# Kernel optimization log

Hardware: AMD Instinct MI355X
Metric: run time of the kernel (lower is better)

The kernel has to match this reference:

```python
import jax, jax.numpy as jnp
import numpy as np

N = 6144       # nodes
E = 98304      # edges (~16 per node)
D = 256        # input_dim
K = 20         # max_clusters
NUM_LVS = 32   # distinct LV group ids
MIN_SIZE = 3.0
MAX_SIZE = 20.0


def _lv_constraint_table():
    # Static per-LV preferred-cluster soft constraint (0.3 base, 1.0 preferred).
    max_cpl = max(2, K // max(1, NUM_LVS - 5))
    table = np.ones((NUM_LVS, K), dtype=np.float32)
    for i in range(NUM_LVS):
        start = (i * 2) % K
        end = min(start + max_cpl, K)
        pref = np.zeros(K, dtype=np.float32)
        pref[start:end] = 1.0
        table[i] = 0.3 + 0.7 * pref
    return jnp.asarray(table)

_LV_TABLE = _lv_constraint_table()


def _apply_size_constraints(S):
    cs = S.sum(axis=0)  # soft cluster sizes [K]
    pen = jnp.zeros_like(cs)
    pen = jnp.where(cs > MAX_SIZE, -jnp.log(cs / MAX_SIZE + 1e-8), pen)
    pen = jnp.where((cs > 0) & (cs < MIN_SIZE), -0.5 * jnp.log(cs / MIN_SIZE + 1e-8), pen)
    S_adj = jax.nn.softmax(jnp.log(S + 1e-8) + pen[None, :], axis=1)
    very_over = cs > MAX_SIZE * 1.5
    for k in range(K):  # K is small & static; sequential like the original
        col = S_adj[:, k]
        thr = jnp.quantile(col, 0.7)
        weak = (col < thr) & very_over[k]
        S_adj = S_adj.at[:, k].set(jnp.where(weak, 0.0, col))
        rs = jnp.sum(jnp.abs(S_adj), axis=1, keepdims=True)
        S_adj = jnp.where(weak[:, None], S_adj / jnp.maximum(rs, 1e-12), S_adj)
    return jnp.where(jnp.any(pen != 0.0), S_adj, S)


def _hard_rebalance(S):
    n = S.shape[0]
    for _ in range(5):  # fixed max_iterations (early-break is a no-op via masks)
        cs = S.sum(axis=0)  # stale within the k-loop, as in the original
        very_over = cs > MAX_SIZE
        for k in range(K):
            excess = cs[k] - MAX_SIZE
            active = very_over[k] & (excess > 0)
            col = S[:, k]
            num = jnp.minimum(jnp.ceil(excess).astype(jnp.int32) + 5, n)
            order = jnp.argsort(col)  # ascending: weakest first
            ranks = jnp.zeros((n,), jnp.int32).at[order].set(jnp.arange(n, dtype=jnp.int32))
            weak = (ranks < num) & active
            S = S.at[:, k].set(jnp.where(weak, 1e-8, col))
            avail = jnp.clip(MAX_SIZE - cs, 0.0, None)
            w = avail / (avail.sum() + 1e-8)
            S = jnp.where(weak[:, None], S + w[None, :] * S[:, k:k + 1], S)
            rs = jnp.sum(jnp.abs(S), axis=1, keepdims=True)
            S = jnp.where(weak[:, None], S / jnp.maximum(rs, 1e-12), S)
    return S


def _forward(x, edge_index, lv_group_ids, W1, b1, W2, b2, W3, b3, We1, be1, We2, be2):
    n = x.shape[0]
    # assign_net (dropout is identity in eval)
    h = jax.nn.relu(x @ W1 + b1)
    h = jax.nn.relu(h @ W2 + b2)
    logits = h @ W3 + b3  # [N, K]

    # LV mask: values in {0.3, 1.0}; masked_fill only triggers on exact zeros (kept faithful)
    lv_sizes = jax.ops.segment_sum(jnp.ones((n,), logits.dtype), lv_group_ids, num_segments=NUM_LVS)
    big = (lv_sizes > 30.0)[lv_group_ids]
    lv_mask = jnp.where(big[:, None], _LV_TABLE[lv_group_ids], 1.0)
    logits = jnp.where(lv_mask == 0.0, -1e9, logits)

    # load-balancing regularization (reconstructed; source truncated)
    S_soft = jax.nn.softmax(logits, axis=1)
    target = n / K
    logits = logits - 0.1 * (S_soft.sum(axis=0) - target)[None, :] / target

    S = jax.nn.softmax(logits, axis=1)
    S = _apply_size_constraints(S)
    S = _hard_rebalance(S)

    x_embed = jax.nn.relu(x @ We1 + be1) @ We2 + be2
    x_pooled = S.T @ x_embed  # [K, D]

    adj = jnp.zeros((n, n), x.dtype).at[edge_index[0], edge_index[1]].set(1.0)
    adj_pooled = S.T @ adj @ S  # [K, K]

    # link prediction loss: BCE(S S^T, adj) with torch's log clamp at -100
    p = jnp.clip(S @ S.T, 0.0, 1.0)
    logp = jnp.maximum(jnp.log(p), -100.0)
    log1mp = jnp.maximum(jnp.log1p(-p), -100.0)
    link_loss = -jnp.mean(adj * logp + (1.0 - adj) * log1mp)

    entropy_loss = -jnp.mean(jnp.sum(S * jnp.log(S + 1e-8), axis=1))
    balance_loss = jnp.mean(jnp.abs(S.sum(axis=0) - target)) / target
    aux = link_loss + 0.1 * entropy_loss + 0.5 * balance_loss
    return x_pooled, adj_pooled, S, aux


def setup_inputs() -> dict:
    key = jax.random.key(0)
    ks = jax.random.split(key, 8)
    x = jax.random.normal(ks[0], (N, D), jnp.float32)
    edge_index = jax.random.randint(ks[1], (2, E), 0, N)
    lv_group_ids = jax.random.randint(ks[2], (N,), 0, NUM_LVS)

    def lin(k, fi, fo):
        k1, k2 = jax.random.split(k)
        lim = 1.0 / np.sqrt(fi)
        return (jax.random.uniform(k1, (fi, fo), jnp.float32, -lim, lim),
                jax.random.uniform(k2, (fo,), jnp.float32, -lim, lim))

    W1, b1 = lin(ks[3], D, D // 2)
    W2, b2 = lin(ks[4], D // 2, D // 4)
    W3 = jax.random.normal(ks[5], (D // 4, K), jnp.float32) * 0.1  # _init_balanced_assignment
    b3 = jnp.zeros((K,), jnp.float32)
    We1, be1 = lin(ks[6], D, D)
    We2, be2 = lin(ks[7], D, D)
    return dict(x=x, edge_index=edge_index, lv_group_ids=lv_group_ids,
                W1=W1, b1=b1, W2=W2, b2=b2, W3=W3, b3=b3,
                We1=We1, be1=be1, We2=We2, be2=be2)


def reference(x, edge_index, lv_group_ids, W1, b1, W2, b2, W3, b3, We1, be1, We2, be2):
    return _forward(x, edge_index, lv_group_ids, W1, b1, W2, b2, W3, b3, We1, be1, We2, be2)
```

## Files before the change

kernel.cpp:

```cpp
#include <hip/hip_runtime.h>
#include <math.h>

#define N_NODES 6144
#define KCL 20
#define NE 98304
#define RPT 6

#define OFF_BITMAP   491520ull
#define OFF_COLSUM0  5210112ull
#define OFF_CSG      5210192ull
#define OFF_CSFIN    5210272ull
#define OFF_DACC     5210368ull
#define OFF_TICK     5210400ull
#define OFF_GBAR2    5210404ull
#define HDR_BYTES    296ull
#define OFF_LOGITS   5210624ull
#define OFF_WEAK     5235200ull
#define OFF_CSS      5358080ull
#define OFF_TOTZ     5358160ull
#define OFF_UCM      5702144ull
#define OFF_XE       6685184ull
#define OFF_GOUT     13001216ull
#define OFF_RWS      13025792ull

__global__ __launch_bounds__(128) void k_mlp(const float* __restrict__ x,
    const float* __restrict__ W1, const float* __restrict__ b1,
    const float* __restrict__ W2, const float* __restrict__ b2,
    const float* __restrict__ W3, const float* __restrict__ b3,
    float* __restrict__ logits, float* __restrict__ colsum0,
    unsigned* __restrict__ bitmap, float* __restrict__ outHead){
  __shared__ float xs[16][256];
  __shared__ float h1[16][128];
  __shared__ float h2[16][64];
  __shared__ float logitsL[16][20];
  __shared__ float csL[20];
  const int tid = threadIdx.x;
  const int r0 = blockIdx.x * 16;
  { uint4* bm4 = (uint4*)bitmap;
    const int base = blockIdx.x*128 + tid;
    const uint4 z = make_uint4(0u,0u,0u,0u);
    #pragma unroll
    for (int i=0;i<6;i++) bm4[base + i*49152] = z; }
  if (blockIdx.x==0){ for (int i=tid;i<5520;i+=128) outHead[i]=0.f; }
  if (tid < 20) csL[tid]=0.f;
  for (int idx = tid; idx < 16*256; idx += 128){ int u = idx >> 8, i = idx & 255; xs[u][i] = x[(r0+u)*256 + i]; }
  __syncthreads();
  {
    float acc[16]; float bb = b1[tid];
    #pragma unroll
    for (int u=0;u<16;u++) acc[u]=bb;
    for (int i=0;i<256;i++){ float wv = W1[i*128+tid];
      #pragma unroll
      for (int u=0;u<16;u++) acc[u]=fmaf(xs[u][i], wv, acc[u]); }
    #pragma unroll
    for (int u=0;u<16;u++) h1[u][tid]=fmaxf(acc[u],0.f);
  }
  __syncthreads();
  if (tid < 64){
    float acc[16]; float bb = b2[tid];
    #pragma unroll
    for (int u=0;u<16;u++) acc[u]=bb;
    for (int i=0;i<128;i++){ float wv = W2[i*64+tid];
      #pragma unroll
      for (int u=0;u<16;u++) acc[u]=fmaf(h1[u][i], wv, acc[u]); }
    #pragma unroll
    for (int u=0;u<16;u++) h2[u][tid]=fmaxf(acc[u],0.f);
  }
  __syncthreads();
  if (tid < 20){
    float acc[16]; float bb = b3[tid];
    #pragma unroll
    for (int u=0;u<16;u++) acc[u]=bb;
    for (int i=0;i<64;i++){ float wv = W3[i*20+tid];
      #pragma unroll
      for (int u=0;u<16;u++) acc[u]=fmaf(h2[u][i], wv, acc[u]); }
    #pragma unroll
    for (int u=0;u<16;u++){ logits[(r0+u)*20+tid]=acc[u]; logitsL[u][tid]=acc[u]; }
  }
  __syncthreads();
  if (tid < 16){
    float y[20]; float m=-INFINITY;
    #pragma unroll
    for (int c=0;c<20;c++){ y[c]=logitsL[tid][c]; m=fmaxf(m,y[c]); }
    float s=0.f;
    #pragma unroll
    for (int c=0;c<20;c++){ y[c]=expf(y[c]-m); s+=y[c]; }
    #pragma unroll
    for (int c=0;c<20;c++) atomicAdd(&csL[c], y[c]/s);
  }
  __syncthreads();
  if (tid < 20) atomicAdd(&colsum0[tid], csL[tid]);
}

__global__ __launch_bounds__(256) void k_sm2p(const float* __restrict__ logits,
    const float* __restrict__ colsum0, float* __restrict__ Ucm,
    float* __restrict__ csG, float* __restrict__ Rws, unsigned* __restrict__ gbar2){
  __shared__ float adjv[20]; __shared__ float csL[20];
  const int tid = threadIdx.x;
  if (tid < 20){ adjv[tid] = (0.1f*(colsum0[tid]-307.2f))/307.2f; csL[tid]=0.f; }
  __syncthreads();
  const int r = blockIdx.x*256 + tid;
  float y[20]; float m=-INFINITY;
  const float4* lp = (const float4*)(logits + r*20);
  #pragma unroll
  for (int q=0;q<5;q++){ float4 f=lp[q]; y[q*4]=f.x; y[q*4+1]=f.y; y[q*4+2]=f.z; y[q*4+3]=f.w; }
  #pragma unroll
  for (int c=0;c<20;c++){ y[c]=y[c]-adjv[c]; m=fmaxf(m,y[c]); }
  float s=0.f;
  #pragma unroll
  for (int c=0;c<20;c++){ y[c]=expf(y[c]-m); s+=y[c]; }
  #pragma unroll
  for (int c=0;c<20;c++){ float v=y[c]/s; y[c]=v; Ucm[c*6144+r]=v; atomicAdd(&csL[c], v); }
  __syncthreads();
  if (tid < 20) atomicAdd(&csG[tid], csL[tid]);
  __syncthreads();
  if (tid==0){
    __threadfence();
    __hip_atomic_fetch_add(gbar2, 1u, __ATOMIC_RELEASE, __HIP_MEMORY_SCOPE_AGENT);
    while (__hip_atomic_load(gbar2, __ATOMIC_ACQUIRE, __HIP_MEMORY_SCOPE_AGENT) < 24u)
      __builtin_amdgcn_s_sleep(2);
    __threadfence();
  }
  __syncthreads();
  float pen[20]; int flag=0;
  #pragma unroll
  for (int c=0;c<20;c++){ float cc=csG[c]; float p=0.f;
    if (cc > 20.0f) p = -logf(cc/20.0f + 1e-8f);
    if (cc > 0.0f && cc < 3.0f) p = -0.5f*logf(cc/3.0f + 1e-8f);
    pen[c]=p; if (p != 0.f) flag=1; }
  float ts=0.f;
  if (flag){
    float m2=-INFINITY;
    #pragma unroll
    for (int c=0;c<20;c++){ y[c]=logf(y[c]+1e-8f)+pen[c]; m2=fmaxf(m2,y[c]); }
    float s2=0.f;
    #pragma unroll
    for (int c=0;c<20;c++){ y[c]=expf(y[c]-m2); s2+=y[c]; }
    #pragma unroll
    for (int c=0;c<20;c++){ float vv=y[c]/s2; Ucm[c*6144+r]=vv; ts+=vv; }
  } else {
    #pragma unroll
    for (int c=0;c<20;c++) ts+=y[c];
  }
  Rws[r]=ts;
}


__device__ __forceinline__ void load6(const float* p, float* v){
  const float2* q = (const float2*)p;
  float2 a=q[0], b=q[1], c=q[2];
  v[0]=a.x; v[1]=a.y; v[2]=b.x; v[3]=b.y; v[4]=c.x; v[5]=c.y;
}

struct MidShared {
  unsigned hist[2048*8];
  unsigned pad[3000];
  double wred[16*20];
  int wT20[16][20]; int wB20[16][20]; int totZ20[20];
  float csGs[20]; float csS[20];
  unsigned st[8];
  alignas(16) unsigned wMin[16];
  alignas(16) int wS[16];
};

__device__ __forceinline__ int blockExclScan16(int val, int tid, int lane, int wv,
                                               int* wS, int* totOut){
  __syncthreads();
  int inc = val;
  for (int off=1;off<64;off<<=1){ int nv=__shfl_up(inc,off); if (lane>=off) inc+=nv; }
  if (lane==63) wS[wv]=inc;
  __syncthreads();
  int4 a=*(int4*)&wS[0], b=*(int4*)&wS[4], c=*(int4*)&wS[8], d=*(int4*)&wS[12];
  int tot = a.x+a.y+a.z+a.w + b.x+b.y+b.z+b.w + c.x+c.y+c.z+c.w + d.x+d.y+d.z+d.w;
  int base = 0;
  base += (wv> 0)?a.x:0; base += (wv> 1)?a.y:0; base += (wv> 2)?a.z:0; base += (wv> 3)?a.w:0;
  base += (wv> 4)?b.x:0; base += (wv> 5)?b.y:0; base += (wv> 6)?b.z:0; base += (wv> 7)?b.w:0;
  base += (wv> 8)?c.x:0; base += (wv> 9)?c.y:0; base += (wv>10)?c.z:0; base += (wv>11)?c.w:0;
  base += (wv>12)?d.x:0; base += (wv>13)?d.y:0; base += (wv>14)?d.z:0;
  *totOut = tot;
  return base + inc - val;
}

struct SelRes { unsigned kv, below, rankin, ties; };

__device__ SelRes selectKth6(const float* v, int rank0, unsigned* hist,
                             unsigned* st, int* wS, int tid, int lane, int wv){
  unsigned st0=0u, st1=0u, st2=(unsigned)rank0, st3=0u;
  const unsigned rep=(unsigned)(lane&7);
  bool done=false;
  for (int p=0;p<3 && !done;p++){
    const int shift=(p==0)?21:((p==1)?10:0);
    const int bins =(p==2)?1024:2048;
    unsigned bb[RPT];
    #pragma unroll
    for (int u=0;u<RPT;u++){
      unsigned key=__float_as_uint(v[u]);
      bool ok=(p==0);
      if (p==1) ok=((key>>21)==(st0>>21));
      if (p==2) ok=((key>>10)==(st0>>10));
      bb[u]= ok ? ((key>>shift)&(unsigned)(bins-1)) : 0xFFFFFFFFu;
    }
    #pragma unroll
    for (int u=0;u<RPT;u++){
      bool first=(bb[u]!=0xFFFFFFFFu);
      #pragma unroll
      for (int j=0;j<u;j++) first = first && (bb[j]!=bb[u]);
      if (first){
        unsigned cnt=1u;
        #pragma unroll
        for (int j=u+1;j<RPT;j++) cnt += (bb[j]==bb[u]) ? 1u:0u;
        atomicAdd(&hist[(bb[u]<<3)+rep], cnt);
      }
    }
    __syncthreads();
    const uint4 z4=make_uint4(0u,0u,0u,0u);
    unsigned bs0, bs1=0u, s;
    const unsigned b0=(unsigned)tid*(unsigned)(bins>>10);
    {
      uint4* h4=(uint4*)&hist[b0<<3];
      uint4 x0=h4[0],x1=h4[1];
      bs0=x0.x+x0.y+x0.z+x0.w + x1.x+x1.y+x1.z+x1.w;
      h4[0]=z4; h4[1]=z4;
      if (bins==2048){
        uint4 x2=h4[2],x3=h4[3];
        bs1=x2.x+x2.y+x2.z+x2.w + x3.x+x3.y+x3.z+x3.w;
        h4[2]=z4; h4[3]=z4;
      }
      s=bs0+bs1;
    }
    unsigned inc=s;
    for (int off=1;off<64;off<<=1){ unsigned nv=(unsigned)__shfl_up((int)inc,off); if (lane>=off) inc+=nv; }
    if (lane==63) wS[wv]=(int)inc;
    __syncthreads();
    int4 wa=*(int4*)&wS[0], wb=*(int4*)&wS[4], wc=*(int4*)&wS[8], wd=*(int4*)&wS[12];
    unsigned base=0u;
    base += (wv> 0)?(unsigned)wa.x:0u; base += (wv> 1)?(unsigned)wa.y:0u;
    base += (wv> 2)?(unsigned)wa.z:0u; base += (wv> 3)?(unsigned)wa.w:0u;
    base += (wv> 4)?(unsigned)wb.x:0u; base += (wv> 5)?(unsigned)wb.y:0u;
    base += (wv> 6)?(unsigned)wb.z:0u; base += (wv> 7)?(unsigned)wb.w:0u;
    base += (wv> 8)?(unsigned)wc.x:0u; base += (wv> 9)?(unsigned)wc.y:0u;
    base += (wv>10)?(unsigned)wc.z:0u; base += (wv>11)?(unsigned)wc.w:0u;
    base += (wv>12)?(unsigned)wd.x:0u; base += (wv>13)?(unsigned)wd.y:0u;
    base += (wv>14)?(unsigned)wd.z:0u;
    unsigned P=base+inc-s;
    if (P<=st2 && st2<P+s){
      unsigned run=P, bsel, hc;
      if (st2 < P+bs0){ bsel=b0;    hc=bs0; }
      else            { run=P+bs0; bsel=b0+1u; hc=bs1; }
      st[0]=st0|(bsel<<(unsigned)shift);
      st[1]=st1+run;
      st[2]=st2-run;
      st[3]=hc;
      st[4]=0xFFFFFFFFu;
      st[5]=0u;
    }
    __syncthreads();
    st0=st[0]; st1=st[1]; st2=st[2]; st3=st[3];
    if (p<2 && st3<=2u){
      #pragma unroll
      for (int u=0;u<RPT;u++){
        unsigned key=__float_as_uint(v[u]);
        if ((key>>(unsigned)shift)==(st0>>(unsigned)shift)){
          atomicMin(&st[4],key); atomicMax(&st[5],key);
        }
      }
      __syncthreads();
      unsigned kmin=st[4], kmax=st[5];
      if (st3==1u)            st0=kmin;
      else if (kmin==kmax)    st0=kmin;
      else if (st2==0u){      st0=kmin; st3=1u; }
      else             {      st0=kmax; st1+=1u; st2=0u; st3=1u; }
      done=true;
    }
  }
  SelRes r; r.kv=st0; r.below=st1; r.rankin=st2; r.ties=st3; return r;
}

__device__ void constr_block(MidShared& sm, const float* __restrict__ csG,
    float* __restrict__ Rws, float* __restrict__ G2, float* __restrict__ Ucm){
  unsigned* hist = sm.hist; unsigned* st = sm.st; int* wS = sm.wS;
  const int tid = threadIdx.x;
  const int lane = tid & 63, wv = tid >> 6;
  const int r0 = tid*RPT;

  { uint4* h4=(uint4*)hist; const uint4 z=make_uint4(0u,0u,0u,0u);
    #pragma unroll
    for (int i=0;i<4;i++) h4[tid+i*1024]=z; }
  if (tid<20) sm.csGs[tid]=csG[tid];
  __syncthreads();

  int flag=0;
  #pragma unroll
  for (int c=0;c<20;c++){ float cc=sm.csGs[c]; float p=0.f;
    if (cc > 20.0f) p = -logf(cc/20.0f + 1e-8f);
    if (cc > 0.0f && cc < 3.0f) p = -0.5f*logf(cc/3.0f + 1e-8f);
    if (p != 0.f) flag=1; }

  float G[RPT], R[RPT];
  load6(Rws + r0, R);
  #pragma unroll
  for (int u=0;u<RPT;u++) G[u]=1.0f;

  if (flag){
    float u24[RPT]; bool have=false;
    for (int k=0;k<20;k++){
      if (!(sm.csGs[k] > 30.0f)){ have=false; continue; }
      if (!have) load6(Ucm + k*6144 + r0, u24);
      float u24n[RPT];
      if (k<19) load6(Ucm + (k+1)*6144 + r0, u24n);
      float sv24[RPT];
      #pragma unroll
      for (int u=0;u<RPT;u++) sv24[u]=__fmul_rn(u24[u], G[u]);
      SelRes sr = selectKth6(sv24, 4300, hist, st, wS, tid, lane, wv);
      float vlo = __uint_as_float(sr.kv);
      float vhi;
      if (sr.rankin + 1u < sr.ties) vhi = vlo;
      else {
        unsigned kV = sr.kv;
        unsigned lm = 0xFFFFFFFFu;
        #pragma unroll
        for (int u=0;u<RPT;u++){ unsigned key=__float_as_uint(sv24[u]); if (key>kV && key<lm) lm=key; }
        for (int off=32;off>0;off>>=1){ unsigned o=(unsigned)__shfl_down((int)lm,off); if (o<lm) lm=o; }
        if (lane==0) sm.wMin[wv]=lm;
        __syncthreads();
        uint4 m0=*(uint4*)&sm.wMin[0], m1=*(uint4*)&sm.wMin[4];
        uint4 m2=*(uint4*)&sm.wMin[8], m3=*(uint4*)&sm.wMin[12];
        lm = m0.x; lm = (m0.y<lm)?m0.y:lm; lm = (m0.z<lm)?m0.z:lm; lm = (m0.w<lm)?m0.w:lm;
        lm = (m1.x<lm)?m1.x:lm; lm = (m1.y<lm)?m1.y:lm; lm = (m1.z<lm)?m1.z:lm; lm = (m1.w<lm)?m1.w:lm;
        lm = (m2.x<lm)?m2.x:lm; lm = (m2.y<lm)?m2.y:lm; lm = (m2.z<lm)?m2.z:lm; lm = (m2.w<lm)?m2.w:lm;
        lm = (m3.x<lm)?m3.x:lm; lm = (m3.y<lm)?m3.y:lm; lm = (m3.z<lm)?m3.z:lm; lm = (m3.w<lm)?m3.w:lm;
        vhi = __uint_as_float(lm);
      }
      float thr = __fadd_rn(__fmul_rn(vlo, 0.89990234375f), __fmul_rn(vhi, 0.10009765625f));
      #pragma unroll
      for (int u=0;u<RPT;u++){
        if (sv24[u] < thr){
          Ucm[k*6144+r0+u] = 0.0f;
          float rs  = __fsub_rn(__fmul_rn(R[u], G[u]), sv24[u]);
          float rsm = fmaxf(rs, 1e-12f);
          G[u] = __fdiv_rn(G[u], rsm);
          R[u] = __fsub_rn(R[u], u24[u]);
        }
      }
      #pragma unroll
      for (int u=0;u<RPT;u++) u24[u]=u24n[u];
      have = (k<19);
    }
  }

  { float2* gp = (float2*)(G2 + r0);
    gp[0]=make_float2(G[0],G[1]); gp[1]=make_float2(G[2],G[3]); gp[2]=make_float2(G[4],G[5]); }
  { float2* rp = (float2*)(Rws + r0);
    rp[0]=make_float2(R[0],R[1]); rp[1]=make_float2(R[2],R[3]); rp[2]=make_float2(R[4],R[5]); }
}

__device__ void embed_block(MidShared& sm, const float* __restrict__ x,
    const float* __restrict__ We1, const float* __restrict__ be1,
    const float* __restrict__ We2, const float* __restrict__ be2,
    float* __restrict__ xe, int blk){
  float (*xs)[256] = (float (*)[256])(sm.hist);
  float (*h)[256]  = (float (*)[256])(sm.hist + 4096);
  const int tid = threadIdx.x;
  const int col = tid & 255;
  const int ug  = tid >> 8;
  const int r0 = blk * 16;
  { float4* xsf4 = (float4*)xs;
    xsf4[tid] = ((const float4*)(x + r0*256))[tid]; }
  __syncthreads();
  float acc[4];
  { float bb = be1[col];
    #pragma unroll
    for (int u=0;u<4;u++) acc[u]=bb; }
  for (int i=0;i<256;i+=4){
    float w0 = We1[(i+0)*256+col];
    float w1 = We1[(i+1)*256+col];
    float w2 = We1[(i+2)*256+col];
    float w3 = We1[(i+3)*256+col];
    #pragma unroll
    for (int u=0;u<4;u++){
      const float4 xv = *(const float4*)&xs[ug*4+u][i];
      acc[u]=fmaf(xv.x, w0, acc[u]);
      acc[u]=fmaf(xv.y, w1, acc[u]);
      acc[u]=fmaf(xv.z, w2, acc[u]);
      acc[u]=fmaf(xv.w, w3, acc[u]);
    }
  }
  #pragma unroll
  for (int u=0;u<4;u++) h[ug*4+u][col]=fmaxf(acc[u],0.f);
  __syncthreads();
  { float bb = be2[col];
    #pragma unroll
    for (int u=0;u<4;u++) acc[u]=bb; }
  for (int i=0;i<256;i+=4){
    float w0 = We2[(i+0)*256+col];
    float w1 = We2[(i+1)*256+col];
    float w2 = We2[(i+2)*256+col];
    float w3 = We2[(i+3)*256+col];
    #pragma unroll
    for (int u=0;u<4;u++){
      const float4 xv = *(const float4*)&h[ug*4+u][i];
      acc[u]=fmaf(xv.x, w0, acc[u]);
      acc[u]=fmaf(xv.y, w1, acc[u]);
      acc[u]=fmaf(xv.z, w2, acc[u]);
      acc[u]=fmaf(xv.w, w3, acc[u]);
    }
  }
  #pragma unroll
  for (int u=0;u<4;u++) xe[(r0+ug*4+u)*256+col]=acc[u];
}

__global__ __launch_bounds__(1024) void k_midwide(const float* __restrict__ csG,
    float* __restrict__ Rws, float* __restrict__ G2,
    float* __restrict__ Ucm,
    const float* __restrict__ x,
    const float* __restrict__ We1, const float* __restrict__ be1,
    const float* __restrict__ We2, const float* __restrict__ be2,
    float* __restrict__ xe,
    const int* __restrict__ ei, unsigned int* __restrict__ bitmap){
  __shared__ MidShared sm;
  const int blk = blockIdx.x;
  if (blk == 0){
    constr_block(sm, csG, Rws, G2, Ucm);
  } else if (blk <= 384){
    embed_block(sm, x, We1, be1, We2, be2, xe, blk-1);
  } else {
    const int e = (blk-385)*1024 + threadIdx.x;
    const int i = ei[e], j = ei[NE+e];
    unsigned bit = (unsigned)i*6144u + (unsigned)j;
    atomicOr(&bitmap[bit >> 5], 1u << (bit & 31u));
  }
}

__global__ __launch_bounds__(1024) void k_rbA(const float* __restrict__ G2,
    const float* __restrict__ Ucm, float* __restrict__ csS, int* __restrict__ totZ,
    unsigned char* __restrict__ weakIt){
  __shared__ double wredL[16];
  __shared__ int wTL[16];
  const int c = blockIdx.x;
  const int tid = threadIdx.x;
  const int lane = tid & 63, wv = tid >> 6;
  const int r0 = tid*RPT;
  float vv[RPT], g[RPT];
  load6(Ucm + c*6144 + r0, vv);
  load6(G2 + r0, g);
  double d=0.0; int z=0;
  #pragma unroll
  for (int u=0;u<RPT;u++){
    if (vv[u]==0.0f) z++;
    d += (double)__fmul_rn(vv[u], g[u]);
  }
  for (int off=32;off>0;off>>=1) d += __shfl_down(d, off);
  int inc=z;
  for (int off=1;off<64;off<<=1){ int nv=__shfl_up(inc,off); if (lane>=off) inc+=nv; }
  if (lane==0)  wredL[wv]=d;
  if (lane==63) wTL[wv]=inc;
  __syncthreads();
  double s=0.0;
  #pragma unroll
  for (int w2=0;w2<16;w2++) s += wredL[w2];
  const float cs=(float)s;
  int base=0, tz=0;
  #pragma unroll
  for (int w2=0;w2<16;w2++){ int t=wTL[w2]; if (w2<wv) base+=t; tz+=t; }
  int num=(int)ceilf(cs-20.0f)+5; if (num>6144) num=6144;
  const bool act = (cs > 20.0f);
  int rank = base + inc - z;
  #pragma unroll
  for (int u=0;u<RPT;u++){
    bool zb = (vv[u]==0.0f);
    unsigned char wi = 255;
    if (act && zb && rank < 5*num) wi = (unsigned char)(rank / num);
    weakIt[c*6144 + r0 + u] = wi;
    if (zb) rank++;
  }
  if (tid==0){ csS[c]=cs; totZ[c]=tz; }
}

__global__ __launch_bounds__(1024) void k_rbB(const float* __restrict__ G2,
    const float* __restrict__ Rws, float* __restrict__ Ucm, float* __restrict__ Gout,
    const float* __restrict__ csS, const int* __restrict__ totZ,
    const unsigned char* __restrict__ weakIt){
  __shared__ MidShared sm;
  const int tid = threadIdx.x;
  float csL[20]; float s0=0.f; unsigned actm=0u;
  #pragma unroll
  for (int c=0;c<20;c++){ float cs=csS[c]; csL[c]=cs;
    s0 += fmaxf(20.0f-cs,0.f);
    if (cs > 20.0f) actm |= (1u<<c); }
  const int wzero=(s0==0.0f)?1:0;
  const float wsum=s0+1e-8f;
  const int anyA=(actm!=0u)?1:0;
  int fastok = wzero;
  #pragma unroll
  for (int c=0;c<20;c++){
    if ((actm>>c)&1u){
      int num=(int)ceilf(csL[c]-20.0f)+5; if (num>6144) num=6144;
      if (5*num > totZ[c]) fastok=0;
    }
  }
  if (!anyA){
    const int r = blockIdx.x*1024 + tid;
    Gout[r] = G2[r];
    return;
  }
  if (fastok){
    const int r = blockIdx.x*1024 + tid;
    float G=G2[r], R=Rws[r];
    unsigned char wi[20];
    #pragma unroll
    for (int c=0;c<20;c++) wi[c]=weakIt[c*6144+r];
    #pragma unroll
    for (int i=0;i<5;i++){
      #pragma unroll
      for (int c=0;c<20;c++){
        if (wi[c]==(unsigned char)i){
          float Gold = G;
          float t   = __fadd_rn(__fmul_rn(R, Gold), 1e-8f);
          float rsm = fmaxf(t, 1e-12f);
          float un  = __fdiv_rn(1e-8f, Gold);
          Ucm[c*6144+r] = un;
          G = __fdiv_rn(Gold, rsm);
          R = __fadd_rn(R, un);
        }
      }
    }
    Gout[r]=G;
  } else {
    if (blockIdx.x!=0) return;
    unsigned* hist = sm.hist; unsigned* st = sm.st; int* wS = sm.wS;
    const int lane = tid & 63, wv = tid >> 6;
    const int r0 = tid*RPT;
    { uint4* h4=(uint4*)hist; const uint4 z=make_uint4(0u,0u,0u,0u);
      #pragma unroll
      for (int i=0;i<4;i++) h4[tid+i*1024]=z; }
    __syncthreads();
    float G[RPT], R[RPT];
    load6(G2 + r0, G);
    load6(Rws + r0, R);
    for (int it=0; it<5; it++){
      int zb2[RPT];
      #pragma unroll
      for (int u=0;u<RPT;u++) zb2[u]=0;
      for (int c=0;c<20;c++){
        float vv[RPT];
        load6(Ucm + c*6144 + r0, vv);
        double d=0.0;
        #pragma unroll
        for (int u=0;u<RPT;u++){
          if (vv[u]==0.0f) zb2[u] |= (1<<c);
          d += (double)__fmul_rn(vv[u], G[u]);
        }
        for (int off=32;off>0;off>>=1) d += __shfl_down(d, off);
        if (lane==0) sm.wred[wv*20+c]=d;
      }
      __syncthreads();
      if (tid<20){ double s=0.0; for (int w2=0;w2<16;w2++) s += sm.wred[w2*20+tid]; sm.csS[tid]=(float)s; }
      __syncthreads();
      float t0=0.f; unsigned am=0u;
      #pragma unroll
      for (int c=0;c<20;c++){
        float cs=sm.csS[c];
        t0 += fmaxf(20.0f-cs,0.f);
        if (cs > 20.0f) am |= (1u<<c);
      }
      const int wz = (t0==0.0f) ? 1 : 0;
      const float ws2 = t0 + 1e-8f;
      int exc2[20];
      #pragma unroll
      for (int c=0;c<20;c++){
        int z=0;
        #pragma unroll
        for (int u=0;u<RPT;u++) z += (zb2[u]>>c)&1;
        int inc = z;
        for (int off=1;off<64;off<<=1){ int nv=__shfl_up(inc,off); if (lane>=off) inc+=nv; }
        if (lane==63) sm.wT20[wv][c]=inc;
        exc2[c]=inc-z;
      }
      __syncthreads();
      if (tid<20){
        int run=0;
        for (int w2=0;w2<16;w2++){ sm.wB20[w2][tid]=run; run+=sm.wT20[w2][tid]; }
        sm.totZ20[tid]=run;
      }
      __syncthreads();
      const int aa = (am!=0u) ? 1 : 0;
      int ng=0;
      #pragma unroll
      for (int c=0;c<20;c++){
        if ((am>>c)&1u){
          float cs=sm.csS[c];
          int num=(int)ceilf(cs-20.0f)+5; if (num>6144) num=6144;
          if (num > sm.totZ20[c]) ng=1;
        }
      }
      if (aa && !wz) ng=1;
      if (!aa) continue;
      if (!ng){
        #pragma unroll
        for (int c=0;c<20;c++){
          if ((am>>c)&1u){
            float cs=sm.csS[c];
            int num=(int)ceilf(cs-20.0f)+5; if (num>6144) num=6144;
            int rank = sm.wB20[wv][c] + exc2[c];
            #pragma unroll
            for (int u=0;u<RPT;u++){
              if ((zb2[u]>>c)&1){
                if (rank < num){
                  float Gold = G[u];
                  float t   = __fadd_rn(__fmul_rn(R[u], Gold), 1e-8f);
                  float rsm = fmaxf(t, 1e-12f);
                  float un  = __fdiv_rn(1e-8f, Gold);
                  Ucm[c*6144+r0+u] = un;
                  G[u] = __fdiv_rn(Gold, rsm);
                  R[u] = __fadd_rn(R[u], un);
                }
                rank++;
              }
            }
          }
        }
      } else {
        for (int k=0;k<20;k++){
          if ((am>>k)&1u){
            float cs=sm.csS[k];
            int num=(int)ceilf(cs-20.0f)+5; if (num>6144) num=6144;
            float u24[RPT];
            load6(Ucm + k*6144 + r0, u24);
            int zc=0;
            #pragma unroll
            for (int u=0;u<RPT;u++) zc += (u24[u]==0.0f) ? 1 : 0;
            int tz2;
            int zBase = blockExclScan16(zc, tid, lane, wv, wS, &tz2);
            bool wk[RPT];
            if (num <= tz2){
              int cnt = zBase;
              #pragma unroll
              for (int u=0;u<RPT;u++){ wk[u]=false; if (u24[u]==0.0f){ if (cnt<num) wk[u]=true; cnt++; } }
            } else {
              float sv24[RPT];
              #pragma unroll
              for (int u=0;u<RPT;u++) sv24[u]=__fmul_rn(u24[u], G[u]);
              SelRes sr = selectKth6(sv24, num-1, hist, st, wS, tid, lane, wv);
              unsigned kV = sr.kv;
              int L = (int)sr.below;
              int Rq = num - L;
              int ec=0;
              #pragma unroll
              for (int u=0;u<RPT;u++) ec += (__float_as_uint(sv24[u])==kV) ? 1 : 0;
              int eTot;
              int eBase = blockExclScan16(ec, tid, lane, wv, wS, &eTot);
              int cnt = eBase;
              #pragma unroll
              for (int u=0;u<RPT;u++){
                unsigned key = __float_as_uint(sv24[u]); wk[u]=false;
                if (key < kV) wk[u]=true;
                else if (key == kV){ if (cnt < Rq) wk[u]=true; cnt++; }
              }
            }
            #pragma unroll
            for (int u=0;u<RPT;u++){
              if (wk[u]){
                const int r = r0+u;
                float rs=0.f; float xv2[20];
                #pragma unroll
                for (int j=0;j<20;j++){
                  float xv = (j==k) ? 1e-8f : __fmul_rn(Ucm[j*6144+r], G[u]);
                  float wLj = fmaxf(20.0f - sm.csS[j], 0.f) / ws2;
                  xv = __fadd_rn(xv, __fmul_rn(wLj, 1e-8f));
                  xv2[j]=xv; rs += fabsf(xv);
                }
                float rsm = fmaxf(rs, 1e-12f);
                float nR = 0.f;
                #pragma unroll
                for (int j=0;j<20;j++){
                  float nv = __fdiv_rn(xv2[j], rsm);
                  Ucm[j*6144+r] = nv; nR += nv;
                }
                G[u]=1.0f; R[u]=nR;
              }
            }
            __syncthreads();
          }
        }
        __syncthreads();
      }
    }
    { float2* gp = (float2*)(Gout + r0);
      gp[0]=make_float2(G[0],G[1]); gp[1]=make_float2(G[2],G[3]); gp[2]=make_float2(G[4],G[5]); }
  }
  (void)wsum;
}

__global__ __launch_bounds__(256) void k_tail1(const float* __restrict__ Ucm,
    const float* __restrict__ Gout, const float* __restrict__ xe,
    const unsigned* __restrict__ bitmap,
    float* __restrict__ outXP, float* __restrict__ outS,
    float* __restrict__ csfin, double* __restrict__ dAcc,
    float* __restrict__ outAdj, float* __restrict__ outAux,
    unsigned* __restrict__ ticket){
  __shared__ float SiT[256][21];
  __shared__ float SjT[256][21];
  __shared__ float csL[20];
  __shared__ float adjacc[400];
  __shared__ double wsum[4];
  const int tid = threadIdx.x;
  const int blk = blockIdx.x;
  const int lane = tid & 63, wvq = tid >> 6;

  if (blk < 24){
    const int r0 = blk * 256;
    if (tid < 20) csL[tid]=0.f;
    __syncthreads();
    {
      const int r = r0 + tid;
      const float Gr = Gout[r];
      float sv[20]; float ent=0.f;
      #pragma unroll
      for (int c=0;c<20;c++) sv[c]=__fmul_rn(Ucm[c*6144+r], Gr);
      float4* so = (float4*)(outS + r*20);
      #pragma unroll
      for (int q=0;q<5;q++){ float4 f; f.x=sv[q*4]; f.y=sv[q*4+1]; f.z=sv[q*4+2]; f.w=sv[q*4+3]; so[q]=f; }
      #pragma unroll
      for (int c=0;c<20;c++){ SiT[tid][c]=sv[c]; ent += sv[c]*logf(sv[c]+1e-08f); }
      #pragma unroll
      for (int c=0;c<20;c++) atomicAdd(&csL[c], sv[c]);
      double ed = (double)ent;
      for (int off=32;off>0;off>>=1) ed += __shfl_down(ed, off);
      if (lane==0) wsum[wvq]=ed;
    }
    __syncthreads();
    if (tid==0) atomicAdd(&dAcc[2], wsum[0]+wsum[1]+wsum[2]+wsum[3]);
    if (tid<20) atomicAdd(&csfin[tid], csL[tid]);
    float acc[20];
    #pragma unroll
    for (int c=0;c<20;c++) acc[c]=0.f;
    for (int i=0;i<256;i++){
      float xv = xe[(r0+i)*256 + tid];
      #pragma unroll
      for (int c=0;c<20;c++) acc[c]=fmaf(SiT[i][c], xv, acc[c]);
    }
    #pragma unroll
    for (int c=0;c<20;c++) atomicAdd(&outXP[c*256+tid], acc[c]);
  } else if (blk < 120){
    const int rbase = (blk-24)*64 + wvq*16;
    for (int t=tid;t<400;t+=256) adjacc[t]=0.f;
    __syncthreads();
    int c7[7], d7[7], n7=0;
    #pragma unroll
    for (int q=0;q<7;q++){ int e=lane+64*q; if (e<400){ c7[q]=e/20; d7[q]=e%20; n7=q+1; } }
    float acc7[7];
    #pragma unroll
    for (int q=0;q<7;q++) acc7[q]=0.f;
    float eacc = 0.f;
    for (int rr=0; rr<16; rr++){
      const int i = rbase + rr;
      const float Gi = Gout[i];
      float Si[20];
      #pragma unroll
      for (int c=0;c<20;c++) Si[c]=__fmul_rn(Ucm[c*6144+i], Gi);
      float Tp[20];
      #pragma unroll
      for (int c=0;c<20;c++) Tp[c]=0.f;
      #pragma unroll
      for (int w=0; w<3; w++){
        const int wq = lane + w*64;
        unsigned word = bitmap[i*192 + wq];
        while (word){
          int b = __ffs((int)word) - 1; word &= (word-1u);
          int j = wq*32 + b;
          const float Gj = Gout[j];
          float p = 0.f;
          #pragma unroll
          for (int c=0;c<20;c++){
            float sj = __fmul_rn(Ucm[c*6144+j], Gj);
            Tp[c] += sj;
            p = fmaf(Si[c], sj, p);
          }
          float pcl = fminf(fmaxf(p,0.f),1.f);
          float lg  = fmaxf(__logf(pcl),      -100.f);
          float l1  = fmaxf(__logf(1.0f-pcl), -100.f);
          eacc += (lg - l1);
        }
      }
      float tr[20];
      #pragma unroll
      for (int c=0;c<20;c++){
        float t = Tp[c];
        for (int off=32;off>0;off>>=1) t += __shfl_xor(t, off);
        tr[c]=t;
      }
      #pragma unroll
      for (int q=0;q<7;q++){
        if (q < n7) acc7[q] = fmaf(Si[c7[q]], tr[d7[q]], acc7[q]);
      }
    }
    #pragma unroll
    for (int q=0;q<7;q++){
      if (q < n7) atomicAdd(&adjacc[lane+64*q], acc7[q]);
    }
    double cd = (double)eacc;
    for (int off=32;off>0;off>>=1) cd += __shfl_down(cd, off);
    if (lane==0) wsum[wvq]=cd;
    __syncthreads();
    if (tid==0) atomicAdd(&dAcc[1], wsum[0]+wsum[1]+wsum[2]+wsum[3]);
    for (int t=tid;t<400;t+=256) atomicAdd(&outAdj[t], adjacc[t]);
  } else {
    const int q2 = blk - 120;
    const int ib = (q2/24)*256, jb = (q2%24)*256;
    const float gi = Gout[ib+tid];
    #pragma unroll
    for (int c=0;c<20;c++) SiT[tid][c] = __fmul_rn(Ucm[c*6144+ib+tid], gi);
    const float gj = Gout[jb+tid];
    #pragma unroll
    for (int c=0;c<20;c++) SjT[tid][c] = __fmul_rn(Ucm[c*6144+jb+tid], gj);
    __syncthreads();
    float rA[20];
    #pragma unroll
    for (int c=0;c<20;c++) rA[c]=SiT[tid][c];
    float af = 0.f;
    for (int jj=0;jj<256;jj++){
      float p=0.f;
      #pragma unroll
      for (int c=0;c<20;c++) p = fmaf(rA[c], SjT[jj][c], p);
      float pcl = fminf(fmaxf(p,0.f),1.f);
      af += fmaxf(__logf(1.0f-pcl), -100.f);
    }
    double cd = (double)af;
    for (int off=32;off>0;off>>=1) cd += __shfl_down(cd, off);
    if (lane==0) wsum[wvq]=cd;
    __syncthreads();
    if (tid==0) atomicAdd(&dAcc[0], wsum[0]+wsum[1]+wsum[2]+wsum[3]);
  }

  __syncthreads();
  if (tid==0){
    unsigned t = atomicAdd(ticket, 1u);
    if (t == 695u){
      __threadfence();
      double l0 = __hip_atomic_load(&dAcc[0], __ATOMIC_RELAXED, __HIP_MEMORY_SCOPE_AGENT);
      double l1 = __hip_atomic_load(&dAcc[1], __ATOMIC_RELAXED, __HIP_MEMORY_SCOPE_AGENT);
      double l2 = __hip_atomic_load(&dAcc[2], __ATOMIC_RELAXED, __HIP_MEMORY_SCOPE_AGENT);
      float s=0.f;
      for (int c=0;c<20;c++){
        float cf = __hip_atomic_load(&csfin[c], __ATOMIC_RELAXED, __HIP_MEMORY_SCOPE_AGENT);
        s += fabsf(cf-307.2f);
      }
      const double nsq = 6144.0*6144.0;
      float link = (float)(-(l0+l1)/nsq);
      float ent  = (float)(-(l2/6144.0));
      float bal = (s/20.0f)/307.2f;
      outAux[0] = link + 0.1f*ent + 0.5f*bal;
    }
  }
}

extern "C" void kernel_launch(void* const* d_in, const int* in_sizes, int n_in,
                              void* d_out, int out_size, void* d_ws, size_t ws_size,
                              hipStream_t stream) {
  const float* x   = (const float*)d_in[0];
  const int*   ei  = (const int*)d_in[1];
  const float* W1  = (const float*)d_in[3];
  const float* b1  = (const float*)d_in[4];
  const float* W2  = (const float*)d_in[5];
  const float* b2  = (const float*)d_in[6];
  const float* W3  = (const float*)d_in[7];
  const float* b3  = (const float*)d_in[8];
  const float* We1 = (const float*)d_in[9];
  const float* be1 = (const float*)d_in[10];
  const float* We2 = (const float*)d_in[11];
  const float* be2 = (const float*)d_in[12];

  char* ws = (char*)d_ws;
  unsigned int* bitmap = (unsigned int*)(ws + OFF_BITMAP);
  float* colsum0  = (float*)(ws + OFF_COLSUM0);
  float* csG      = (float*)(ws + OFF_CSG);
  float* csfin    = (float*)(ws + OFF_CSFIN);
  double* dAcc    = (double*)(ws + OFF_DACC);
  unsigned* ticket= (unsigned*)(ws + OFF_TICK);
  unsigned* gbar2 = (unsigned*)(ws + OFF_GBAR2);
  float* logits   = (float*)(ws + OFF_LOGITS);
  float* Ucm      = (float*)(ws + OFF_UCM);
  float* xe       = (float*)(ws + OFF_XE);
  float* Gout     = (float*)(ws + OFF_GOUT);
  float* Rws      = (float*)(ws + OFF_RWS);
  float* G2       = logits;
  unsigned char* weakIt = (unsigned char*)(ws + OFF_WEAK);
  float* csS      = (float*)(ws + OFF_CSS);
  int*   totZ     = (int*)(ws + OFF_TOTZ);

  float* out   = (float*)d_out;
  float* outXP = out;
  float* outAdj= out + 5120;
  float* outS  = out + 5520;
  float* outAux= out + 128400;

  hipMemsetAsync(ws + OFF_COLSUM0, 0, (size_t)HDR_BYTES, stream);

  k_mlp<<<384, 128, 0, stream>>>(x, W1,b1, W2,b2, W3,b3, logits, colsum0, bitmap, out);
  k_sm2p<<<24, 256, 0, stream>>>(logits, colsum0, Ucm, csG, Rws, gbar2);
  k_midwide<<<481, 1024, 0, stream>>>(csG, Rws, G2, Ucm,
                                      x, We1, be1, We2, be2, xe, ei, bitmap);
  k_rbA<<<20, 1024, 0, stream>>>(G2, Ucm, csS, totZ, weakIt);
  k_rbB<<<6, 1024, 0, stream>>>(G2, Rws, Ucm, Gout, csS, totZ, weakIt);
  k_tail1<<<696, 256, 0, stream>>>(Ucm, Gout, xe, bitmap,
                                   outXP, outS, csfin, dAcc, outAdj, outAux, ticket);
}
```

Before: 508.0 us.

## Fuse rebalance kernels into midwide launch with flag-based inter-block waits

```diff
diff --git a/kernel.cpp b/kernel.cpp
--- a/kernel.cpp
+++ b/kernel.cpp
@@ -13,7 +13,9 @@
 #define OFF_DACC     5210368ull
 #define OFF_TICK     5210400ull
 #define OFF_GBAR2    5210404ull
-#define HDR_BYTES    296ull
+#define OFF_FLAGC    5210408ull
+#define OFF_RBAD     5210412ull
+#define HDR_BYTES    304ull
 #define OFF_LOGITS   5210624ull
 #define OFF_WEAK     5235200ull
 #define OFF_CSS      5358080ull
@@ -277,7 +279,8 @@
 }
 
 __device__ void constr_block(MidShared& sm, const float* __restrict__ csG,
-    float* __restrict__ Rws, float* __restrict__ G2, float* __restrict__ Ucm){
+    float* __restrict__ Rws, float* __restrict__ G2, float* __restrict__ Ucm,
+    unsigned* __restrict__ flagC){
   unsigned* hist = sm.hist; unsigned* st = sm.st; int* wS = sm.wS;
   const int tid = threadIdx.x;
   const int lane = tid & 63, wv = tid >> 6;
@@ -352,6 +355,11 @@
     gp[0]=make_float2(G[0],G[1]); gp[1]=make_float2(G[2],G[3]); gp[2]=make_float2(G[4],G[5]); }
   { float2* rp = (float2*)(Rws + r0);
     rp[0]=make_float2(R[0],R[1]); rp[1]=make_float2(R[2],R[3]); rp[2]=make_float2(R[4],R[5]); }
+  __syncthreads();
+  if (tid==0){
+    __threadfence();
+    __hip_atomic_store(flagC, 1u, __ATOMIC_RELEASE, __HIP_MEMORY_SCOPE_AGENT);
+  }
 }
 
 __device__ void embed_block(MidShared& sm, const float* __restrict__ x,
@@ -409,37 +417,19 @@
   for (int u=0;u<4;u++) xe[(r0+ug*4+u)*256+col]=acc[u];
 }
 
-__global__ __launch_bounds__(1024) void k_midwide(const float* __restrict__ csG,
-    float* __restrict__ Rws, float* __restrict__ G2,
-    float* __restrict__ Ucm,
-    const float* __restrict__ x,
-    const float* __restrict__ We1, const float* __restrict__ be1,
-    const float* __restrict__ We2, const float* __restrict__ be2,
-    float* __restrict__ xe,
-    const int* __restrict__ ei, unsigned int* __restrict__ bitmap){
-  __shared__ MidShared sm;
-  const int blk = blockIdx.x;
-  if (blk == 0){
-    constr_block(sm, csG, Rws, G2, Ucm);
-  } else if (blk <= 384){
-    embed_block(sm, x, We1, be1, We2, be2, xe, blk-1);
-  } else {
-    const int e = (blk-385)*1024 + threadIdx.x;
-    const int i = ei[e], j = ei[NE+e];
-    unsigned bit = (unsigned)i*6144u + (unsigned)j;
-    atomicOr(&bitmap[bit >> 5], 1u << (bit & 31u));
-  }
-}
-
-__global__ __launch_bounds__(1024) void k_rbA(const float* __restrict__ G2,
+__device__ void rbA_block(MidShared& sm, const float* __restrict__ G2,
     const float* __restrict__ Ucm, float* __restrict__ csS, int* __restrict__ totZ,
-    unsigned char* __restrict__ weakIt){
-  __shared__ double wredL[16];
-  __shared__ int wTL[16];
-  const int c = blockIdx.x;
+    unsigned char* __restrict__ weakIt, unsigned* __restrict__ flagC,
+    unsigned* __restrict__ rbad, int c){
   const int tid = threadIdx.x;
   const int lane = tid & 63, wv = tid >> 6;
   const int r0 = tid*RPT;
+  if (tid==0){
+    while (__hip_atomic_load(flagC, __ATOMIC_ACQUIRE, __HIP_MEMORY_SCOPE_AGENT) == 0u)
+      __builtin_amdgcn_s_sleep(8);
+    __threadfence();
+  }
+  __syncthreads();
   float vv[RPT], g[RPT];
   load6(Ucm + c*6144 + r0, vv);
   load6(G2 + r0, g);
@@ -452,16 +442,16 @@
   for (int off=32;off>0;off>>=1) d += __shfl_down(d, off);
   int inc=z;
   for (int off=1;off<64;off<<=1){ int nv=__shfl_up(inc,off); if (lane>=off) inc+=nv; }
-  if (lane==0)  wredL[wv]=d;
-  if (lane==63) wTL[wv]=inc;
+  if (lane==0)  sm.wred[wv]=d;
+  if (lane==63) sm.wS[wv]=inc;
   __syncthreads();
   double s=0.0;
   #pragma unroll
-  for (int w2=0;w2<16;w2++) s += wredL[w2];
+  for (int w2=0;w2<16;w2++) s += sm.wred[w2];
   const float cs=(float)s;
   int base=0, tz=0;
   #pragma unroll
-  for (int w2=0;w2<16;w2++){ int t=wTL[w2]; if (w2<wv) base+=t; tz+=t; }
+  for (int w2=0;w2<16;w2++){ int t=sm.wS[w2]; if (w2<wv) base+=t; tz+=t; }
   int num=(int)ceilf(cs-20.0f)+5; if (num>6144) num=6144;
   const bool act = (cs > 20.0f);
   int rank = base + inc - z;
@@ -474,14 +464,24 @@
     if (zb) rank++;
   }
   if (tid==0){ csS[c]=cs; totZ[c]=tz; }
-}
-
-__global__ __launch_bounds__(1024) void k_rbB(const float* __restrict__ G2,
+  __syncthreads();
+  if (tid==0){
+    __threadfence();
+    __hip_atomic_fetch_add(rbad, 1u, __ATOMIC_RELEASE, __HIP_MEMORY_SCOPE_AGENT);
+  }
+}
+
+__device__ void rbB_block(MidShared& sm, const float* __restrict__ G2,
     const float* __restrict__ Rws, float* __restrict__ Ucm, float* __restrict__ Gout,
     const float* __restrict__ csS, const int* __restrict__ totZ,
-    const unsigned char* __restrict__ weakIt){
-  __shared__ MidShared sm;
+    const unsigned char* __restrict__ weakIt, unsigned* __restrict__ rbad, int blk2){
   const int tid = threadIdx.x;
+  if (tid==0){
+    while (__hip_atomic_load(rbad, __ATOMIC_ACQUIRE, __HIP_MEMORY_SCOPE_AGENT) < 20u)
+      __builtin_amdgcn_s_sleep(8);
+    __threadfence();
+  }
+  __syncthreads();
   float csL[20]; float s0=0.f; unsigned actm=0u;
   #pragma unroll
   for (int c=0;c<20;c++){ float cs=csS[c]; csL[c]=cs;
@@ -499,12 +499,12 @@
     }
   }
   if (!anyA){
-    const int r = blockIdx.x*1024 + tid;
+    const int r = blk2*1024 + tid;
     Gout[r] = G2[r];
     return;
   }
   if (fastok){
-    const int r = blockIdx.x*1024 + tid;
+    const int r = blk2*1024 + tid;
     float G=G2[r], R=Rws[r];
     unsigned char wi[20];
     #pragma unroll
@@ -526,7 +526,7 @@
     }
     Gout[r]=G;
   } else {
-    if (blockIdx.x!=0) return;
+    if (blk2!=0) return;
     unsigned* hist = sm.hist; unsigned* st = sm.st; int* wS = sm.wS;
     const int lane = tid & 63, wv = tid >> 6;
     const int r0 = tid*RPT;
@@ -691,6 +691,35 @@
   (void)wsum;
 }
 
+__global__ __launch_bounds__(1024) void k_midwide(const float* __restrict__ csG,
+    float* __restrict__ Rws, float* __restrict__ G2,
+    float* __restrict__ Ucm,
+    const float* __restrict__ x,
+    const float* __restrict__ We1, const float* __restrict__ be1,
+    const float* __restrict__ We2, const float* __restrict__ be2,
+    float* __restrict__ xe,
+    const int* __restrict__ ei, unsigned int* __restrict__ bitmap,
+    float* __restrict__ csS, int* __restrict__ totZ,
+    unsigned char* __restrict__ weakIt, float* __restrict__ Gout,
+    unsigned* __restrict__ flagC, unsigned* __restrict__ rbad){
+  __shared__ MidShared sm;
+  const int blk = blockIdx.x;
+  if (blk == 0){
+    constr_block(sm, csG, Rws, G2, Ucm, flagC);
+  } else if (blk <= 384){
+    embed_block(sm, x, We1, be1, We2, be2, xe, blk-1);
+  } else if (blk <= 480){
+    const int e = (blk-385)*1024 + threadIdx.x;
+    const int i = ei[e], j = ei[NE+e];
+    unsigned bit = (unsigned)i*6144u + (unsigned)j;
+    atomicOr(&bitmap[bit >> 5], 1u << (bit & 31u));
+  } else if (blk <= 500){
+    rbA_block(sm, G2, Ucm, csS, totZ, weakIt, flagC, rbad, blk-481);
+  } else {
+    rbB_block(sm, G2, Rws, Ucm, Gout, csS, totZ, weakIt, rbad, blk-501);
+  }
+}
+
 __global__ __launch_bounds__(256) void k_tail1(const float* __restrict__ Ucm,
     const float* __restrict__ Gout, const float* __restrict__ xe,
     const unsigned* __restrict__ bitmap,
@@ -878,6 +907,8 @@
   double* dAcc    = (double*)(ws + OFF_DACC);
   unsigned* ticket= (unsigned*)(ws + OFF_TICK);
   unsigned* gbar2 = (unsigned*)(ws + OFF_GBAR2);
+  unsigned* flagC = (unsigned*)(ws + OFF_FLAGC);
+  unsigned* rbad  = (unsigned*)(ws + OFF_RBAD);
   float* logits   = (float*)(ws + OFF_LOGITS);
   float* Ucm      = (float*)(ws + OFF_UCM);
   float* xe       = (float*)(ws + OFF_XE);
@@ -898,10 +929,9 @@
 
   k_mlp<<<384, 128, 0, stream>>>(x, W1,b1, W2,b2, W3,b3, logits, colsum0, bitmap, out);
   k_sm2p<<<24, 256, 0, stream>>>(logits, colsum0, Ucm, csG, Rws, gbar2);
-  k_midwide<<<481, 1024, 0, stream>>>(csG, Rws, G2, Ucm,
-                                      x, We1, be1, We2, be2, xe, ei, bitmap);
-  k_rbA<<<20, 1024, 0, stream>>>(G2, Ucm, csS, totZ, weakIt);
-  k_rbB<<<6, 1024, 0, stream>>>(G2, Rws, Ucm, Gout, csS, totZ, weakIt);
+  k_midwide<<<507, 1024, 0, stream>>>(csG, Rws, G2, Ucm,
+                                      x, We1, be1, We2, be2, xe, ei, bitmap,
+                                      csS, totZ, weakIt, Gout, flagC, rbad);
   k_tail1<<<696, 256, 0, stream>>>(Ucm, Gout, xe, bitmap,
                                    outXP, outS, csfin, dAcc, outAdj, outAux, ticket);
 }
```

After: 476.5 us. -6.2%, faster.
